# Optimization experiments

Measured on AMD Instinct MI355X. Metric: run time of the kernel, lower is better.

The kernel has to match this reference:

```python
import jax, jax.numpy as jnp
import numpy as np

B, L, C = 2, 2048, 1024
H, DK = 16, 64  # multiNum, dk
EPS = 1e-5
MASK_VAL = -2**15 + 1  # matches masked_fill value in torch source


def layer_norm(x, g, b):
    mu = jnp.mean(x, axis=-1, keepdims=True)
    var = jnp.var(x, axis=-1, keepdims=True)
    return (x - mu) * jax.lax.rsqrt(var + EPS) * g + b


def setup_inputs() -> dict:
    key = jax.random.key(0)
    ks = jax.random.split(key, 12)
    s_in = 1.0 / np.sqrt(C)
    s_attn = 1.0 / np.sqrt(H * DK)
    return {
        "qx": jax.random.normal(ks[0], (B, L, C), jnp.float32),
        "kx": jax.random.normal(ks[1], (B, L, C), jnp.float32),
        "vx": jax.random.normal(ks[2], (B, L, C), jnp.float32),
        "maskPAD": jax.random.randint(ks[3], (B, L, L), 0, 2, jnp.int32),
        "ln_g": jnp.ones((C,), jnp.float32),
        "ln_b": jnp.zeros((C,), jnp.float32),
        "wq": jax.random.uniform(ks[4], (C, H * DK), jnp.float32, -s_in, s_in),
        "bq": jax.random.uniform(ks[5], (H * DK,), jnp.float32, -s_in, s_in),
        "wk": jax.random.uniform(ks[6], (C, H * DK), jnp.float32, -s_in, s_in),
        "bk": jax.random.uniform(ks[7], (H * DK,), jnp.float32, -s_in, s_in),
        "wv": jax.random.uniform(ks[8], (C, H * DK), jnp.float32, -s_in, s_in),
        "bv": jax.random.uniform(ks[9], (H * DK,), jnp.float32, -s_in, s_in),
        "wo": jax.random.uniform(ks[10], (H * DK, C), jnp.float32, -s_attn, s_attn),
        "bo": jax.random.uniform(ks[11], (C,), jnp.float32, -s_attn, s_attn),
    }


def reference(qx, kx, vx, maskPAD, ln_g, ln_b, wq, bq, wk, bk, wv, bv, wo, bo):
    # PreLN with shared LayerNorm params across q/k/v (as in source)
    qn = layer_norm(qx, ln_g, ln_b)
    kn = layer_norm(kx, ln_g, ln_b)
    vn = layer_norm(vx, ln_g, ln_b)
    # project and split heads: [B, H, L, DK]
    q = (qn @ wq + bq).reshape(B, L, H, DK).transpose(0, 2, 1, 3)
    k = (kn @ wk + bk).reshape(B, L, H, DK).transpose(0, 2, 1, 3)
    v = (vn @ wv + bv).reshape(B, L, H, DK).transpose(0, 2, 1, 3)
    scores = jnp.einsum("bhqd,bhkd->bhqk", q, k) / np.sqrt(DK).astype(np.float32)
    scores = jnp.where((maskPAD == 0)[:, None, :, :], jnp.float32(MASK_VAL), scores)
    alpha = jax.nn.softmax(scores, axis=-1)
    z = jnp.einsum("bhqk,bhkd->bhqd", alpha, v)
    z = z.transpose(0, 2, 1, 3).reshape(B, L, H * DK)
    return z @ wo + bo
```

## Files before the change

### kernel.cpp

```cpp
#include <hip/hip_runtime.h>
#include <hip/hip_bf16.h>

#define B_ 2
#define L_ 2048
#define C_ 1024
#define H_ 16
#define DK_ 64
#define M_ (B_*L_)
#define MASK_VALF (-32767.0f)
#define LOG2E 1.44269504088896f

typedef __attribute__((ext_vector_type(8))) short bf16x8;
typedef __attribute__((ext_vector_type(4))) float f32x4;
typedef __attribute__((ext_vector_type(4))) unsigned uint4v;

static __device__ __forceinline__ short f2bf(float f) {
    __hip_bfloat16 h = __float2bfloat16(f);
    return *reinterpret_cast<short*>(&h);
}

static __device__ __forceinline__ float exp2_raw(float x) {
    float r;
    asm("v_exp_f32 %0, %1" : "=v"(r) : "v"(x));
    return r;
}
static __device__ __forceinline__ unsigned cvt_pk_bf16(float lo, float hi) {
    unsigned r;
    asm("v_cvt_pk_bf16_f32 %0, %1, %2" : "=v"(r) : "v"(lo), "v"(hi));
    return r;
}

__global__ __launch_bounds__(256) void ln_kernel(
    const float* __restrict__ qx, const float* __restrict__ kx, const float* __restrict__ vx,
    const float* __restrict__ g, const float* __restrict__ bias,
    short* __restrict__ qn, short* __restrict__ kn, short* __restrict__ vn)
{
    const int row = blockIdx.x;
    const int which = blockIdx.y;
    const float* src = (which == 0) ? qx : (which == 1) ? kx : vx;
    short* dst = (which == 0) ? qn : (which == 1) ? kn : vn;
    src += (size_t)row * C_;
    dst += (size_t)row * C_;
    const int t = threadIdx.x;
    float4 xv = reinterpret_cast<const float4*>(src)[t];
    float s  = xv.x + xv.y + xv.z + xv.w;
    float s2 = xv.x*xv.x + xv.y*xv.y + xv.z*xv.z + xv.w*xv.w;
    #pragma unroll
    for (int off = 32; off > 0; off >>= 1) {
        s  += __shfl_down(s, off);
        s2 += __shfl_down(s2, off);
    }
    __shared__ float red[8];
    const int wid = t >> 6, lane = t & 63;
    if (lane == 0) { red[wid] = s; red[4 + wid] = s2; }
    __syncthreads();
    const float ts  = red[0] + red[1] + red[2] + red[3];
    const float ts2 = red[4] + red[5] + red[6] + red[7];
    const float mu  = ts * (1.0f / C_);
    const float var = ts2 * (1.0f / C_) - mu * mu;
    const float rs  = rsqrtf(var + 1e-5f);
    float4 gv = reinterpret_cast<const float4*>(g)[t];
    float4 bv = reinterpret_cast<const float4*>(bias)[t];
    short4 o;
    o.x = f2bf((xv.x - mu) * rs * gv.x + bv.x);
    o.y = f2bf((xv.y - mu) * rs * gv.y + bv.y);
    o.z = f2bf((xv.z - mu) * rs * gv.z + bv.z);
    o.w = f2bf((xv.w - mu) * rs * gv.w + bv.w);
    reinterpret_cast<short4*>(dst)[t] = o;
}

__global__ void wconv_kernel(
    const float* __restrict__ wq, const float* __restrict__ wk,
    const float* __restrict__ wv, const float* __restrict__ wo,
    short* __restrict__ wqt, short* __restrict__ wkt,
    short* __restrict__ wvt, short* __restrict__ wot)
{
    const int mz = blockIdx.z;
    const float* w = (mz==0)?wq:(mz==1)?wk:(mz==2)?wv:wo;
    short* wt = (mz==0)?wqt:(mz==1)?wkt:(mz==2)?wvt:wot;
    __shared__ float tile[32][33];
    const int tx = threadIdx.x, ty = threadIdx.y;
    const int k0 = blockIdx.x * 32, n0 = blockIdx.y * 32;
    #pragma unroll
    for (int r = 0; r < 4; r++) {
        const int k = k0 + ty + r*8;
        tile[ty + r*8][tx] = w[(size_t)k * 1024 + n0 + tx];
    }
    __syncthreads();
    #pragma unroll
    for (int r = 0; r < 4; r++) {
        const int n = n0 + ty + r*8;
        wt[(size_t)n * 1024 + k0 + tx] = f2bf(tile[tx][ty + r*8]);
    }
}

__global__ __launch_bounds__(256) void maskpack_kernel(
    const int* __restrict__ mask, unsigned long long* __restrict__ bits)
{
    const int gw = blockIdx.x * 4 + (threadIdx.x >> 6);
    const int lane = threadIdx.x & 63;
    const int k = (gw & 31) * 64 + lane;
    const int rowq = gw >> 5;
    const int v = mask[(size_t)rowq * L_ + k];
    unsigned long long bal = __ballot(v != 0);
    if (lane == 0) bits[gw] = bal;
}

__device__ __forceinline__ void gemm_core_128(
    const short* __restrict__ Abf, const short* __restrict__ Bt,
    int m0, int n0, short* lds, f32x4 (&acc)[4][4])
{
    const int t = threadIdx.x, w = t >> 6, l = t & 63;
    const int wm = w >> 1, wn = w & 1;
    const int l15 = l & 15, l4 = l >> 4;
    const int srow = t >> 2, scol = (t & 3) * 8;
    const short* aS = Abf + (size_t)(m0 + srow) * 1024 + scol;
    const short* bS = Bt  + (size_t)(n0 + srow) * 1024 + scol;
    char* lb = (char*)lds;
    const int wb = w * 1024;

    #define GSTAGE(buf, kt) do {                                                   \
        const int ko = (kt) * 32;                                                  \
        char* dst = lb + (buf)*16384;                                              \
        __builtin_amdgcn_global_load_lds(                                          \
            (const __attribute__((address_space(1))) void*)(aS + ko),              \
            (__attribute__((address_space(3))) void*)(dst + wb), 16, 0, 0);        \
        __builtin_amdgcn_global_load_lds(                                          \
            (const __attribute__((address_space(1))) void*)(aS + 64*1024 + ko),    \
            (__attribute__((address_space(3))) void*)(dst + wb + 4096), 16, 0, 0); \
        __builtin_amdgcn_global_load_lds(                                          \
            (const __attribute__((address_space(1))) void*)(bS + ko),              \
            (__attribute__((address_space(3))) void*)(dst + 8192 + wb), 16, 0, 0); \
        __builtin_amdgcn_global_load_lds(                                          \
            (const __attribute__((address_space(1))) void*)(bS + 64*1024 + ko),    \
            (__attribute__((address_space(3))) void*)(dst + 8192 + wb + 4096), 16, 0, 0); \
    } while (0)

    GSTAGE(0, 0);
    for (int kt = 0; kt < 32; ++kt) {
        __syncthreads();
        if (kt + 1 < 32) GSTAGE((kt + 1) & 1, kt + 1);
        const short* Lb = lds + (kt & 1) * 8192;
        bf16x8 af[4], bfr[4];
        #pragma unroll
        for (int fm = 0; fm < 4; fm++)
            af[fm] = *reinterpret_cast<const bf16x8*>(&Lb[(wm*64 + fm*16 + l15)*32 + l4*8]);
        #pragma unroll
        for (int fn = 0; fn < 4; fn++)
            bfr[fn] = *reinterpret_cast<const bf16x8*>(&Lb[4096 + (wn*64 + fn*16 + l15)*32 + l4*8]);
        #pragma unroll
        for (int fm = 0; fm < 4; fm++)
            #pragma unroll
            for (int fn = 0; fn < 4; fn++)
                acc[fm][fn] = __builtin_amdgcn_mfma_f32_16x16x32_bf16(af[fm], bfr[fn], acc[fm][fn], 0, 0, 0);
    }
    #undef GSTAGE
}

__global__ __launch_bounds__(256) void gemm_proj(
    const short* __restrict__ qn, const short* __restrict__ kn, const short* __restrict__ vn,
    const short* __restrict__ wqt, const short* __restrict__ wkt, const short* __restrict__ wvt,
    const float* __restrict__ bq, const float* __restrict__ bk, const float* __restrict__ bv,
    short* __restrict__ qb, short* __restrict__ kb, short* __restrict__ vtb)
{
    const int pi = blockIdx.y;
    const short* Abf = (pi==0)?qn:(pi==1)?kn:vn;
    const short* Bt  = (pi==0)?wqt:(pi==1)?wkt:wvt;
    const float* bias= (pi==0)?bq:(pi==1)?bk:bv;
    short* outp      = (pi==0)?qb:(pi==1)?kb:vtb;
    const float scale = (pi==0)?(0.125f*LOG2E):1.0f;

    __shared__ short lds[16384];
    const int bx = blockIdx.x;
    const int m0 = (bx >> 3) * 128, n0 = (bx & 7) * 128;
    f32x4 acc[4][4] = {};
    gemm_core_128(Abf, Bt, m0, n0, lds, acc);

    const int t = threadIdx.x, w = t >> 6, l = t & 63;
    const int wm = w >> 1, wn = w & 1, l15 = l & 15, l4 = l >> 4;
    #pragma unroll
    for (int fn = 0; fn < 4; fn++) {
        const int col = n0 + wn*64 + fn*16 + l15;
        const float bsv = bias[col];
        const int h = col >> 6, dk = col & 63;
        #pragma unroll
        for (int fm = 0; fm < 4; fm++) {
            const int row0 = m0 + wm*64 + fm*16 + l4*4;
            const int bb = row0 >> 11, lr0 = row0 & (L_ - 1);
            if (pi == 2) {
                const int lrp = (lr0 & ~63) | ((fm >> 1)*32 + l4*8 + (fm & 1)*4);
                short4 s4;
                #pragma unroll
                for (int r = 0; r < 4; r++)
                    ((short*)&s4)[r] = f2bf(acc[fm][fn][r] + bsv);
                *reinterpret_cast<short4*>(
                    &outp[(((size_t)bb*H_ + h)*DK_ + dk)*L_ + lrp]) = s4;
            } else {
                #pragma unroll
                for (int r = 0; r < 4; r++) {
                    const float vvf = (acc[fm][fn][r] + bsv) * scale;
                    outp[(((size_t)bb*H_ + h)*L_ + lr0 + r)*DK_ + dk] = f2bf(vvf);
                }
            }
        }
    }
}

__global__ __launch_bounds__(256) void gemm_out_k(
    const short* __restrict__ zb, const short* __restrict__ wot,
    const float* __restrict__ bo, float* __restrict__ out)
{
    __shared__ short lds[12288];
    const int t = threadIdx.x, w = t >> 6, l = t & 63;
    const int wm = w >> 1, wn = w & 1;
    const int l15 = l & 15, l4 = l >> 4;
    const int bx = blockIdx.x;
    const int m0 = (bx >> 3) * 64, n0 = (bx & 7) * 128;

    const int srow = l >> 2, scol = (l & 3) * 8;
    const short* aS = zb  + (size_t)(m0 + w*16 + srow) * 1024 + scol;
    const short* bS = wot + (size_t)(n0 + w*32 + srow) * 1024 + scol;
    char* lb = (char*)lds;

    f32x4 acc[2][4] = {};

    #define OSTAGE(buf, kt) do {                                                    \
        const int ko = (kt) * 32;                                                   \
        char* dst = lb + (buf)*12288;                                               \
        __builtin_amdgcn_global_load_lds(                                           \
            (const __attribute__((address_space(1))) void*)(aS + ko),               \
            (__attribute__((address_space(3))) void*)(dst + w*1024), 16, 0, 0);     \
        __builtin_amdgcn_global_load_lds(                                           \
            (const __attribute__((address_space(1))) void*)(bS + ko),               \
            (__attribute__((address_space(3))) void*)(dst + 4096 + w*2048), 16, 0, 0); \
        __builtin_amdgcn_global_load_lds(                                           \
            (const __attribute__((address_space(1))) void*)(bS + 16*1024 + ko),     \
            (__attribute__((address_space(3))) void*)(dst + 4096 + w*2048 + 1024), 16, 0, 0); \
    } while (0)

    OSTAGE(0, 0);
    for (int kt = 0; kt < 32; ++kt) {
        __syncthreads();
        if (kt + 1 < 32) OSTAGE((kt + 1) & 1, kt + 1);
        const short* Lb = lds + (kt & 1) * 6144;
        bf16x8 af[2], bfr[4];
        #pragma unroll
        for (int fm = 0; fm < 2; fm++)
            af[fm] = *reinterpret_cast<const bf16x8*>(&Lb[(wm*32 + fm*16 + l15)*32 + l4*8]);
        #pragma unroll
        for (int fn = 0; fn < 4; fn++)
            bfr[fn] = *reinterpret_cast<const bf16x8*>(&Lb[2048 + (wn*64 + fn*16 + l15)*32 + l4*8]);
        #pragma unroll
        for (int fm = 0; fm < 2; fm++)
            #pragma unroll
            for (int fn = 0; fn < 4; fn++)
                acc[fm][fn] = __builtin_amdgcn_mfma_f32_16x16x32_bf16(af[fm], bfr[fn], acc[fm][fn], 0, 0, 0);
    }
    #undef OSTAGE

    #pragma unroll
    for (int fn = 0; fn < 4; fn++) {
        const int col = n0 + wn*64 + fn*16 + l15;
        const float bsv = bo[col];
        #pragma unroll
        for (int fm = 0; fm < 2; fm++) {
            #pragma unroll
            for (int r = 0; r < 4; r++) {
                const int row = m0 + wm*32 + fm*16 + l4*4 + r;
                out[(size_t)row * C_ + col] = acc[fm][fn][r] + bsv;
            }
        }
    }
}

__global__ __launch_bounds__(512) void attn_kernel(
    const short* __restrict__ qbuf, const short* __restrict__ kbuf, const short* __restrict__ vt,
    const unsigned long long* __restrict__ mbits, short* __restrict__ zb)
{
    __shared__ short Kt[2][64*64];
    __shared__ short Vt[2][64*64];
    const int t = threadIdx.x, w = t >> 6, l = t & 63;
    const int l15 = l & 15, l4 = l >> 4;
    const int bid = blockIdx.x;
    const int bh = bid & 31, qb = bid >> 5;
    const int qt0 = qb * 128;
    const int b = bh >> 4, h = bh & 15;
    const size_t base  = (size_t)bh * L_ * DK_;
    const size_t vbase = (size_t)bh * DK_ * L_;

    const int q = qt0 + w*16 + l15;

    const int srow = w*8 + (l >> 3);
    const int scolb = ((l & 7) * 16) ^ ((srow & 7) << 4);

    bf16x8 qf[2];
    #pragma unroll
    for (int kk = 0; kk < 2; kk++)
        qf[kk] = *reinterpret_cast<const bf16x8*>(&qbuf[base + (size_t)q*DK_ + kk*32 + l4*8]);

    const uint2* mb32 = reinterpret_cast<const uint2*>(mbits + ((size_t)b*L_ + q) * (L_/64));

    f32x4 oacc[4];
    #pragma unroll
    for (int nt = 0; nt < 4; nt++) oacc[nt] = (f32x4){0.f, 0.f, 0.f, 0.f};
    f32x4 lacc = (f32x4){0.f, 0.f, 0.f, 0.f};

    uint4v onesu = {0x3F803F80u, 0x3F803F80u, 0x3F803F80u, 0x3F803F80u};
    const bf16x8 onesv = *reinterpret_cast<const bf16x8*>(&onesu);

    #define STAGE(buf, kt) do {                                                      \
        const int k0s = (kt) * 64;                                                   \
        const char* gk = (const char*)(kbuf + base + (size_t)(k0s + srow)*DK_) + scolb; \
        __builtin_amdgcn_global_load_lds(                                            \
            (const __attribute__((address_space(1))) void*)gk,                       \
            (__attribute__((address_space(3))) void*)((char*)&Kt[buf][0] + w*1024), 16, 0, 0); \
        const char* gv = (const char*)(vt + vbase + (size_t)srow*L_ + k0s) + scolb;  \
        __builtin_amdgcn_global_load_lds(                                            \
            (const __attribute__((address_space(1))) void*)gv,                       \
            (__attribute__((address_space(3))) void*)((char*)&Vt[buf][0] + w*1024), 16, 0, 0); \
    } while (0)

    const int sw = (l15 & 7) << 4;

    auto body = [&](const char* Kb, const char* Vb, unsigned mlo, unsigned mhi) {
        f32x4 sfr[4];
        #pragma unroll
        for (int ct = 0; ct < 4; ct++) {
            const int krow = ct*16 + l15;
            bf16x8 kf0 = *reinterpret_cast<const bf16x8*>(Kb + krow*128 + ((l4*16) ^ sw));
            bf16x8 kf1 = *reinterpret_cast<const bf16x8*>(Kb + krow*128 + ((64 + l4*16) ^ sw));
            f32x4 a = (f32x4){0.f, 0.f, 0.f, 0.f};
            a = __builtin_amdgcn_mfma_f32_16x16x32_bf16(kf0, qf[0], a, 0, 0, 0);
            a = __builtin_amdgcn_mfma_f32_16x16x32_bf16(kf1, qf[1], a, 0, 0, 0);
            sfr[ct] = a;
        }

        unsigned pu[8];
        #pragma unroll
        for (int ct = 0; ct < 4; ct++) {
            const unsigned nib = (((ct < 2) ? mlo : mhi) >> ((ct & 1)*16 + l4*4)) & 0xFu;
            float p[4];
            #pragma unroll
            for (int r = 0; r < 4; r++) {
                const float s = (nib & (1u << r)) ? sfr[ct][r] : MASK_VALF;
                p[r] = exp2_raw(s);
            }
            pu[ct*2]     = cvt_pk_bf16(p[0], p[1]);
            pu[ct*2 + 1] = cvt_pk_bf16(p[2], p[3]);
        }

        uint4v a0 = {pu[0], pu[1], pu[2], pu[3]};
        uint4v a1 = {pu[4], pu[5], pu[6], pu[7]};
        const bf16x8 af0 = *reinterpret_cast<const bf16x8*>(&a0);
        const bf16x8 af1 = *reinterpret_cast<const bf16x8*>(&a1);

        lacc = __builtin_amdgcn_mfma_f32_16x16x32_bf16(af0, onesv, lacc, 0, 0, 0);
        lacc = __builtin_amdgcn_mfma_f32_16x16x32_bf16(af1, onesv, lacc, 0, 0, 0);

        #pragma unroll
        for (int nt = 0; nt < 4; nt++) {
            const int vrow = nt*16 + l15;
            bf16x8 vf0 = *reinterpret_cast<const bf16x8*>(Vb + vrow*128 + ((l4*16) ^ sw));
            bf16x8 vf1 = *reinterpret_cast<const bf16x8*>(Vb + vrow*128 + ((64 + l4*16) ^ sw));
            oacc[nt] = __builtin_amdgcn_mfma_f32_16x16x32_bf16(af0, vf0, oacc[nt], 0, 0, 0);
            oacc[nt] = __builtin_amdgcn_mfma_f32_16x16x32_bf16(af1, vf1, oacc[nt], 0, 0, 0);
        }
    };

    const char* K0 = (const char*)&Kt[0][0];
    const char* K1 = (const char*)&Kt[1][0];
    const char* V0 = (const char*)&Vt[0][0];
    const char* V1 = (const char*)&Vt[1][0];

    STAGE(0, 0);
    uint2 mwv = mb32[0], mwn;

    for (int kt = 0; kt < L_/64; kt += 2) {
        __syncthreads();
        STAGE(1, kt + 1);
        mwn = mb32[kt + 1];
        body(K0, V0, mwv.x, mwv.y);
        mwv = mwn;
        __syncthreads();
        if (kt + 2 < L_/64) { STAGE(0, kt + 2); mwn = mb32[kt + 2]; }
        body(K1, V1, mwv.x, mwv.y);
        mwv = mwn;
    }
    #undef STAGE

    #pragma unroll
    for (int nt = 0; nt < 4; nt++) {
        #pragma unroll
        for (int r = 0; r < 4; r++) {
            const int qg = qt0 + w*16 + l4*4 + r;
            const float ov = oacc[nt][r] / lacc[r];
            zb[((size_t)b*L_ + qg)*C_ + h*DK_ + nt*16 + l15] = f2bf(ov);
        }
    }
}

extern "C" void kernel_launch(void* const* d_in, const int* in_sizes, int n_in,
                              void* d_out, int out_size, void* d_ws, size_t ws_size,
                              hipStream_t stream)
{
    (void)in_sizes; (void)n_in; (void)out_size; (void)ws_size;
    const float* qx = (const float*)d_in[0];
    const float* kx = (const float*)d_in[1];
    const float* vx = (const float*)d_in[2];
    const int*   mp = (const int*)d_in[3];
    const float* lg = (const float*)d_in[4];
    const float* lbt= (const float*)d_in[5];
    const float* wq = (const float*)d_in[6];
    const float* bq = (const float*)d_in[7];
    const float* wk = (const float*)d_in[8];
    const float* bk = (const float*)d_in[9];
    const float* wv = (const float*)d_in[10];
    const float* bv = (const float*)d_in[11];
    const float* wo = (const float*)d_in[12];
    const float* bo = (const float*)d_in[13];
    float* out = (float*)d_out;

    short* ws0 = (short*)d_ws;
    short* qn  = ws0;
    short* kn  = qn + (size_t)M_*C_;
    short* vn  = kn + (size_t)M_*C_;
    short* wqt = vn + (size_t)M_*C_;
    short* wkt = wqt + 1024*1024;
    short* wvt = wkt + 1024*1024;
    short* wot = wvt + 1024*1024;
    short* qbuf = wot + 1024*1024;
    short* kbuf = qbuf + (size_t)M_*C_;
    short* vtb  = kbuf + (size_t)M_*C_;
    short* zbuf = vtb + (size_t)M_*C_;
    unsigned long long* mbits = (unsigned long long*)(zbuf + (size_t)M_*C_);

    hipLaunchKernelGGL(ln_kernel, dim3(M_, 3), dim3(256), 0, stream,
                       qx, kx, vx, lg, lbt, qn, kn, vn);
    hipLaunchKernelGGL(wconv_kernel, dim3(32, 32, 4), dim3(32, 8), 0, stream,
                       wq, wk, wv, wo, wqt, wkt, wvt, wot);
    hipLaunchKernelGGL(maskpack_kernel, dim3((B_*L_*L_/64)/4), dim3(256), 0, stream,
                       mp, mbits);
    hipLaunchKernelGGL(gemm_proj, dim3(256, 3), dim3(256), 0, stream,
                       qn, kn, vn, wqt, wkt, wvt, bq, bk, bv, qbuf, kbuf, vtb);
    hipLaunchKernelGGL(attn_kernel, dim3(512), dim3(512), 0, stream,
                       qbuf, kbuf, vtb, mbits, zbuf);
    hipLaunchKernelGGL(gemm_out_k, dim3(512), dim3(256), 0, stream,
                       zbuf, wot, bo, out);
}
```

Measured before the change: 144.5 us.

## Process two query tiles per wave in attention to reuse K/V fragments

The attention kernel now uses 4 waves (256 threads) per block instead of 8. Each wave handles 32 query rows as two 16-row groups that share the K and V fragments read from LDS. Staging is split into two passes per wave so the same 64x64 K/V tiles are still filled. This halves LDS fragment reads per MFMA and the number of waves contending at the barriers, at the cost of doubling accumulator and score registers per wave, which may lower occupancy.

After: 151.2 us. 1.05x slower.

```diff
diff --git a/kernel.cpp b/kernel.cpp
--- a/kernel.cpp
+++ b/kernel.cpp
@@ -273,7 +273,7 @@
     }
 }
 
-__global__ __launch_bounds__(512) void attn_kernel(
+__global__ __launch_bounds__(256) void attn_kernel(
     const short* __restrict__ qbuf, const short* __restrict__ kbuf, const short* __restrict__ vt,
     const unsigned long long* __restrict__ mbits, short* __restrict__ zb)
 {
@@ -288,82 +288,107 @@
     const size_t base  = (size_t)bh * L_ * DK_;
     const size_t vbase = (size_t)bh * DK_ * L_;
 
-    const int q = qt0 + w*16 + l15;
-
     const int srow = w*8 + (l >> 3);
-    const int scolb = ((l & 7) * 16) ^ ((srow & 7) << 4);
-
-    bf16x8 qf[2];
-    #pragma unroll
-    for (int kk = 0; kk < 2; kk++)
-        qf[kk] = *reinterpret_cast<const bf16x8*>(&qbuf[base + (size_t)q*DK_ + kk*32 + l4*8]);
-
-    const uint2* mb32 = reinterpret_cast<const uint2*>(mbits + ((size_t)b*L_ + q) * (L_/64));
-
-    f32x4 oacc[4];
-    #pragma unroll
-    for (int nt = 0; nt < 4; nt++) oacc[nt] = (f32x4){0.f, 0.f, 0.f, 0.f};
-    f32x4 lacc = (f32x4){0.f, 0.f, 0.f, 0.f};
+    const int scolb0 = (l & 7) * 16;
+
+    bf16x8 qf[2][2];
+    #pragma unroll
+    for (int g = 0; g < 2; g++) {
+        const int qg = qt0 + w*32 + g*16 + l15;
+        #pragma unroll
+        for (int kk = 0; kk < 2; kk++)
+            qf[g][kk] = *reinterpret_cast<const bf16x8*>(
+                &qbuf[base + (size_t)qg*DK_ + kk*32 + l4*8]);
+    }
+
+    const uint2* mbA = reinterpret_cast<const uint2*>(
+        mbits + ((size_t)b*L_ + qt0 + w*32 + l15) * (L_/64));
+    const uint2* mbB = reinterpret_cast<const uint2*>(
+        mbits + ((size_t)b*L_ + qt0 + w*32 + 16 + l15) * (L_/64));
+
+    f32x4 oacc[2][4];
+    #pragma unroll
+    for (int g = 0; g < 2; g++)
+        #pragma unroll
+        for (int nt = 0; nt < 4; nt++) oacc[g][nt] = (f32x4){0.f, 0.f, 0.f, 0.f};
+    f32x4 lacc[2];
+    lacc[0] = (f32x4){0.f, 0.f, 0.f, 0.f};
+    lacc[1] = (f32x4){0.f, 0.f, 0.f, 0.f};
 
     uint4v onesu = {0x3F803F80u, 0x3F803F80u, 0x3F803F80u, 0x3F803F80u};
     const bf16x8 onesv = *reinterpret_cast<const bf16x8*>(&onesu);
 
     #define STAGE(buf, kt) do {                                                      \
         const int k0s = (kt) * 64;                                                   \
-        const char* gk = (const char*)(kbuf + base + (size_t)(k0s + srow)*DK_) + scolb; \
-        __builtin_amdgcn_global_load_lds(                                            \
-            (const __attribute__((address_space(1))) void*)gk,                       \
-            (__attribute__((address_space(3))) void*)((char*)&Kt[buf][0] + w*1024), 16, 0, 0); \
-        const char* gv = (const char*)(vt + vbase + (size_t)srow*L_ + k0s) + scolb;  \
-        __builtin_amdgcn_global_load_lds(                                            \
-            (const __attribute__((address_space(1))) void*)gv,                       \
-            (__attribute__((address_space(3))) void*)((char*)&Vt[buf][0] + w*1024), 16, 0, 0); \
+        _Pragma("unroll")                                                            \
+        for (int p = 0; p < 2; p++) {                                                \
+            const int row = p*32 + srow;                                             \
+            const int colb = scolb0 ^ ((row & 7) << 4);                              \
+            const char* gk = (const char*)(kbuf + base + (size_t)(k0s + row)*DK_) + colb; \
+            __builtin_amdgcn_global_load_lds(                                        \
+                (const __attribute__((address_space(1))) void*)gk,                   \
+                (__attribute__((address_space(3))) void*)((char*)&Kt[buf][0] + p*4096 + w*1024), 16, 0, 0); \
+            const char* gv = (const char*)(vt + vbase + (size_t)row*L_ + k0s) + colb; \
+            __builtin_amdgcn_global_load_lds(                                        \
+                (const __attribute__((address_space(1))) void*)gv,                   \
+                (__attribute__((address_space(3))) void*)((char*)&Vt[buf][0] + p*4096 + w*1024), 16, 0, 0); \
+        }                                                                            \
     } while (0)
 
     const int sw = (l15 & 7) << 4;
 
-    auto body = [&](const char* Kb, const char* Vb, unsigned mlo, unsigned mhi) {
-        f32x4 sfr[4];
+    auto body = [&](const char* Kb, const char* Vb, uint2 mwA, uint2 mwB) {
+        f32x4 sfr[2][4];
         #pragma unroll
         for (int ct = 0; ct < 4; ct++) {
             const int krow = ct*16 + l15;
             bf16x8 kf0 = *reinterpret_cast<const bf16x8*>(Kb + krow*128 + ((l4*16) ^ sw));
             bf16x8 kf1 = *reinterpret_cast<const bf16x8*>(Kb + krow*128 + ((64 + l4*16) ^ sw));
-            f32x4 a = (f32x4){0.f, 0.f, 0.f, 0.f};
-            a = __builtin_amdgcn_mfma_f32_16x16x32_bf16(kf0, qf[0], a, 0, 0, 0);
-            a = __builtin_amdgcn_mfma_f32_16x16x32_bf16(kf1, qf[1], a, 0, 0, 0);
-            sfr[ct] = a;
-        }
-
-        unsigned pu[8];
-        #pragma unroll
-        for (int ct = 0; ct < 4; ct++) {
-            const unsigned nib = (((ct < 2) ? mlo : mhi) >> ((ct & 1)*16 + l4*4)) & 0xFu;
-            float p[4];
-            #pragma unroll
-            for (int r = 0; r < 4; r++) {
-                const float s = (nib & (1u << r)) ? sfr[ct][r] : MASK_VALF;
-                p[r] = exp2_raw(s);
-            }
-            pu[ct*2]     = cvt_pk_bf16(p[0], p[1]);
-            pu[ct*2 + 1] = cvt_pk_bf16(p[2], p[3]);
-        }
-
-        uint4v a0 = {pu[0], pu[1], pu[2], pu[3]};
-        uint4v a1 = {pu[4], pu[5], pu[6], pu[7]};
-        const bf16x8 af0 = *reinterpret_cast<const bf16x8*>(&a0);
-        const bf16x8 af1 = *reinterpret_cast<const bf16x8*>(&a1);
-
-        lacc = __builtin_amdgcn_mfma_f32_16x16x32_bf16(af0, onesv, lacc, 0, 0, 0);
-        lacc = __builtin_amdgcn_mfma_f32_16x16x32_bf16(af1, onesv, lacc, 0, 0, 0);
+            #pragma unroll
+            for (int g = 0; g < 2; g++) {
+                f32x4 a = (f32x4){0.f, 0.f, 0.f, 0.f};
+                a = __builtin_amdgcn_mfma_f32_16x16x32_bf16(kf0, qf[g][0], a, 0, 0, 0);
+                a = __builtin_amdgcn_mfma_f32_16x16x32_bf16(kf1, qf[g][1], a, 0, 0, 0);
+                sfr[g][ct] = a;
+            }
+        }
+
+        bf16x8 af0[2], af1[2];
+        #pragma unroll
+        for (int g = 0; g < 2; g++) {
+            const unsigned mlo = g ? mwB.x : mwA.x;
+            const unsigned mhi = g ? mwB.y : mwA.y;
+            unsigned pu[8];
+            #pragma unroll
+            for (int ct = 0; ct < 4; ct++) {
+                const unsigned nib = (((ct < 2) ? mlo : mhi) >> ((ct & 1)*16 + l4*4)) & 0xFu;
+                float p[4];
+                #pragma unroll
+                for (int r = 0; r < 4; r++) {
+                    const float s = (nib & (1u << r)) ? sfr[g][ct][r] : MASK_VALF;
+                    p[r] = exp2_raw(s);
+                }
+                pu[ct*2]     = cvt_pk_bf16(p[0], p[1]);
+                pu[ct*2 + 1] = cvt_pk_bf16(p[2], p[3]);
+            }
+            uint4v a0 = {pu[0], pu[1], pu[2], pu[3]};
+            uint4v a1 = {pu[4], pu[5], pu[6], pu[7]};
+            af0[g] = *reinterpret_cast<const bf16x8*>(&a0);
+            af1[g] = *reinterpret_cast<const bf16x8*>(&a1);
+            lacc[g] = __builtin_amdgcn_mfma_f32_16x16x32_bf16(af0[g], onesv, lacc[g], 0, 0, 0);
+            lacc[g] = __builtin_amdgcn_mfma_f32_16x16x32_bf16(af1[g], onesv, lacc[g], 0, 0, 0);
+        }
 
         #pragma unroll
         for (int nt = 0; nt < 4; nt++) {
             const int vrow = nt*16 + l15;
             bf16x8 vf0 = *reinterpret_cast<const bf16x8*>(Vb + vrow*128 + ((l4*16) ^ sw));
             bf16x8 vf1 = *reinterpret_cast<const bf16x8*>(Vb + vrow*128 + ((64 + l4*16) ^ sw));
-            oacc[nt] = __builtin_amdgcn_mfma_f32_16x16x32_bf16(af0, vf0, oacc[nt], 0, 0, 0);
-            oacc[nt] = __builtin_amdgcn_mfma_f32_16x16x32_bf16(af1, vf1, oacc[nt], 0, 0, 0);
+            #pragma unroll
+            for (int g = 0; g < 2; g++) {
+                oacc[g][nt] = __builtin_amdgcn_mfma_f32_16x16x32_bf16(af0[g], vf0, oacc[g][nt], 0, 0, 0);
+                oacc[g][nt] = __builtin_amdgcn_mfma_f32_16x16x32_bf16(af1[g], vf1, oacc[g][nt], 0, 0, 0);
+            }
         }
     };
 
@@ -373,28 +398,31 @@
     const char* V1 = (const char*)&Vt[1][0];
 
     STAGE(0, 0);
-    uint2 mwv = mb32[0], mwn;
+    uint2 mA = mbA[0], mB = mbB[0], mAn, mBn;
 
     for (int kt = 0; kt < L_/64; kt += 2) {
         __syncthreads();
         STAGE(1, kt + 1);
-        mwn = mb32[kt + 1];
-        body(K0, V0, mwv.x, mwv.y);
-        mwv = mwn;
+        mAn = mbA[kt + 1]; mBn = mbB[kt + 1];
+        body(K0, V0, mA, mB);
+        mA = mAn; mB = mBn;
         __syncthreads();
-        if (kt + 2 < L_/64) { STAGE(0, kt + 2); mwn = mb32[kt + 2]; }
-        body(K1, V1, mwv.x, mwv.y);
-        mwv = mwn;
+        if (kt + 2 < L_/64) { STAGE(0, kt + 2); mAn = mbA[kt + 2]; mBn = mbB[kt + 2]; }
+        body(K1, V1, mA, mB);
+        mA = mAn; mB = mBn;
     }
     #undef STAGE
 
     #pragma unroll
-    for (int nt = 0; nt < 4; nt++) {
-        #pragma unroll
-        for (int r = 0; r < 4; r++) {
-            const int qg = qt0 + w*16 + l4*4 + r;
-            const float ov = oacc[nt][r] / lacc[r];
-            zb[((size_t)b*L_ + qg)*C_ + h*DK_ + nt*16 + l15] = f2bf(ov);
+    for (int g = 0; g < 2; g++) {
+        #pragma unroll
+        for (int nt = 0; nt < 4; nt++) {
+            #pragma unroll
+            for (int r = 0; r < 4; r++) {
+                const int qg = qt0 + w*32 + g*16 + l4*4 + r;
+                const float ov = oacc[g][nt][r] / lacc[g][r];
+                zb[((size_t)b*L_ + qg)*C_ + h*DK_ + nt*16 + l15] = f2bf(ov);
+            }
         }
     }
 }
@@ -442,7 +470,7 @@
                        mp, mbits);
     hipLaunchKernelGGL(gemm_proj, dim3(256, 3), dim3(256), 0, stream,
                        qn, kn, vn, wqt, wkt, wvt, bq, bk, bv, qbuf, kbuf, vtb);
-    hipLaunchKernelGGL(attn_kernel, dim3(512), dim3(512), 0, stream,
+    hipLaunchKernelGGL(attn_kernel, dim3(512), dim3(256), 0, stream,
                        qbuf, kbuf, vtb, mbits, zbuf);
     hipLaunchKernelGGL(gemm_out_k, dim3(512), dim3(256), 0, stream,
                        zbuf, wot, bo, out);
```
